# Kernel optimization log

Hardware: AMD Instinct MI355X
Metric: run time of the kernel (lower is better)

Reference implementation:

```python
import jax, jax.numpy as jnp
import numpy as np

KS = 3      # kernel_size
PAD = 1     # zero padding applied to x before sampling
STRIDE = 1  # stride of p_conv and final conv (as written in the repo)


def conv2d(x, w, b=None, stride=1, padding=0):
    out = jax.lax.conv_general_dilated(
        x, w, (stride, stride), [(padding, padding), (padding, padding)],
        dimension_numbers=("NCHW", "OIHW", "NCHW"))
    if b is not None:
        out = out + b[None, :, None, None]
    return out


def setup_inputs() -> dict:
    key = jax.random.key(0)
    k1, k2, k3, k4 = jax.random.split(key, 4)
    bsz, inc, outc, H, W = 4, 64, 128, 128, 128
    N = KS * KS
    x = jax.random.normal(k1, (bsz, inc, H, W), dtype=jnp.float32)
    # p_conv: Conv2d(inc, 2*ks*ks, 3, padding=1) with bias (small weights -> modest offsets)
    w_p = jax.random.normal(k2, (2 * N, inc, 3, 3), dtype=jnp.float32) * 0.02
    b_p = jax.random.normal(k3, (2 * N,), dtype=jnp.float32) * 0.1
    # final conv: Conv2d(inc, outc, ks, stride=stride, bias=None)
    w_conv = jax.random.normal(k4, (outc, inc, KS, KS), dtype=jnp.float32) * 0.05
    return {"x": x, "w_p": w_p, "b_p": b_p, "w_conv": w_conv}


def deform_conv_forward(x, w_p, b_p, w_conv):
    ks, pad, stride = KS, PAD, STRIDE
    offset = conv2d(x, w_p, b_p, stride=stride, padding=1)  # (b, 2N, oh, ow)
    N = offset.shape[1] // 2
    bsz, c, _, _ = x.shape
    oh, ow = offset.shape[2], offset.shape[3]
    xp = jnp.pad(x, ((0, 0), (0, 0), (pad, pad), (pad, pad)))
    Hp, Wp = xp.shape[2], xp.shape[3]

    # p_n: kernel-grid offsets, order matches torch.meshgrid 'ij' then flatten
    r = jnp.arange(-(ks - 1) // 2, (ks - 1) // 2 + 1, dtype=x.dtype)
    pnx, pny = jnp.meshgrid(r, r, indexing="ij")
    p_n = jnp.concatenate([pnx.ravel(), pny.ravel()])[None, :, None, None]  # (1,2N,1,1)

    # p_0: base sampling coordinates (1-indexed into padded image)
    i0 = jnp.arange(1, oh * stride + 1, stride, dtype=x.dtype)
    j0 = jnp.arange(1, ow * stride + 1, stride, dtype=x.dtype)
    p0x = jnp.broadcast_to(i0[:, None], (oh, ow))[None, None]
    p0y = jnp.broadcast_to(j0[None, :], (oh, ow))[None, None]
    p_0 = jnp.concatenate([jnp.tile(p0x, (1, N, 1, 1)), jnp.tile(p0y, (1, N, 1, 1))], axis=1)

    p = (p_0 + p_n + offset).transpose(0, 2, 3, 1)  # (b, oh, ow, 2N)

    q_lt_f = jnp.floor(p)
    q_rb_f = q_lt_f + 1.0

    def clamp_q(q):
        return jnp.concatenate(
            [jnp.clip(q[..., :N], 0, Hp - 1), jnp.clip(q[..., N:], 0, Wp - 1)],
            axis=-1).astype(jnp.int32)

    q_lt = clamp_q(q_lt_f)
    q_rb = clamp_q(q_rb_f)
    q_lb = jnp.concatenate([q_lt[..., :N], q_rb[..., N:]], axis=-1)
    q_rt = jnp.concatenate([q_rb[..., :N], q_lt[..., N:]], axis=-1)

    # clamp p itself (indices are detached in torch; gradients flow only through p here)
    p = jnp.concatenate(
        [jnp.clip(p[..., :N], 0, Hp - 1), jnp.clip(p[..., N:], 0, Wp - 1)], axis=-1)
    px, py = p[..., :N], p[..., N:]

    qf = lambda q: q.astype(x.dtype)
    g_lt = (1 + (qf(q_lt[..., :N]) - px)) * (1 + (qf(q_lt[..., N:]) - py))
    g_rb = (1 - (qf(q_rb[..., :N]) - px)) * (1 - (qf(q_rb[..., N:]) - py))
    g_lb = (1 + (qf(q_lb[..., :N]) - px)) * (1 - (qf(q_lb[..., N:]) - py))
    g_rt = (1 - (qf(q_rt[..., :N]) - px)) * (1 + (qf(q_rt[..., N:]) - py))

    x_flat = xp.reshape(bsz, c, Hp * Wp)

    def get_x_q(q):
        idx = q[..., :N] * Wp + q[..., N:]                     # (b, oh, ow, N)
        idxf = jnp.broadcast_to(idx.reshape(bsz, 1, -1), (bsz, c, oh * ow * N))
        return jnp.take_along_axis(x_flat, idxf, axis=2).reshape(bsz, c, oh, ow, N)

    x_off = (g_lt[:, None] * get_x_q(q_lt) + g_rb[:, None] * get_x_q(q_rb)
             + g_lb[:, None] * get_x_q(q_lb) + g_rt[:, None] * get_x_q(q_rt))

    # _reshape_x_offset: (b,c,oh,ow,ks*ks) -> (b,c,oh*ks,ow*ks)
    x_off = x_off.reshape(bsz, c, oh, ow, ks, ks).transpose(0, 1, 2, 4, 3, 5)
    x_off = x_off.reshape(bsz, c, oh * ks, ow * ks)

    return conv2d(x_off, w_conv, None, stride=stride, padding=0)


def reference(x, w_p, b_p, w_conv):
    return deform_conv_forward(x, w_p, b_p, w_conv)
```

## Files before the change

kernel.cpp:

```cpp
#include <hip/hip_runtime.h>
#include <hip/hip_bf16.h>

#define B_   4
#define IC   64
#define OC   128
#define HH   128
#define WW   128
#define HP   130
#define XOF  384
#define XPAD 388
#define OH2  382

typedef __attribute__((ext_vector_type(4))) float f32x4;
typedef __attribute__((ext_vector_type(8))) __bf16 bf16x8;
typedef __attribute__((ext_vector_type(8))) unsigned short us8;
typedef __attribute__((ext_vector_type(4), aligned(4))) float f32x4u;

__device__ __forceinline__ void gload16(const void* gsrc, void* ldst) {
    __builtin_amdgcn_global_load_lds(
        (const __attribute__((address_space(1))) void*)gsrc,
        (__attribute__((address_space(3))) void*)ldst, 16, 0, 0);
}

#define WAITV(N) asm volatile("s_waitcnt vmcnt(" #N ")" ::: "memory")

__global__ __launch_bounds__(256) void nchw2nhwc(const float* __restrict__ x,
                                                 float* __restrict__ xt) {
    __shared__ float tile[64][33];
    int bid = blockIdx.x;
    int xt4 = bid & 3;
    int y   = (bid >> 2) & 127;
    int b   = bid >> 9;
    int x0  = xt4 * 32;

    int t  = threadIdx.x;
    int xl = t & 31;
    int c8 = t >> 5;
#pragma unroll
    for (int it = 0; it < 8; ++it) {
        int c = it * 8 + c8;
        tile[c][xl] = x[(((size_t)b * IC + c) * HH + y) * WW + x0 + xl];
    }
    __syncthreads();
    int c  = t & 63;
    int xw = t >> 6;
#pragma unroll
    for (int it = 0; it < 8; ++it) {
        int xx = it * 4 + xw;
        xt[(((size_t)b * HH + y) * WW + x0 + xx) * IC + c] = tile[c][xx];
    }
}

__global__ __launch_bounds__(256) void offset_lds4(const float* __restrict__ x,
                                                   const float* __restrict__ w_p,
                                                   const float* __restrict__ b_p,
                                                   float* __restrict__ off) {
    __shared__ float part[4][64][18];

    int t   = threadIdx.x;
    int pxl = t & 63;
    int icq = t >> 6;
    int seg = blockIdx.x & 1;
    int row = blockIdx.x >> 1;
    int py  = row & 127;
    int b   = row >> 7;
    int px  = seg * 64 + pxl;
    int ic0 = __builtin_amdgcn_readfirstlane(icq << 4);

    float acc[18];
#pragma unroll
    for (int co = 0; co < 18; ++co) acc[co] = 0.f;

    const float* xb = x + ((size_t)b * IC + ic0) * HH * WW;

    for (int ci = 0; ci < 16; ++ci) {
        const float* xc = xb + (size_t)ci * HH * WW;
        float xv[9];
#pragma unroll
        for (int ky = 0; ky < 3; ++ky) {
            int yy = py + ky - 1;
            bool yok = (yy >= 0) && (yy < HH);
#pragma unroll
            for (int kx = 0; kx < 3; ++kx) {
                int xx = px + kx - 1;
                bool ok = yok && (xx >= 0) && (xx < WW);
                xv[ky * 3 + kx] = ok ? xc[yy * WW + xx] : 0.f;
            }
        }
#pragma unroll
        for (int co = 0; co < 18; ++co) {
            const float* wrow = w_p + ((size_t)co * IC + ic0 + ci) * 9;
            f32x4u w0 = *(const f32x4u*)wrow;
            f32x4u w1 = *(const f32x4u*)(wrow + 4);
            float  w8 = wrow[8];
            acc[co] = fmaf(w0.x, xv[0], acc[co]);
            acc[co] = fmaf(w0.y, xv[1], acc[co]);
            acc[co] = fmaf(w0.z, xv[2], acc[co]);
            acc[co] = fmaf(w0.w, xv[3], acc[co]);
            acc[co] = fmaf(w1.x, xv[4], acc[co]);
            acc[co] = fmaf(w1.y, xv[5], acc[co]);
            acc[co] = fmaf(w1.z, xv[6], acc[co]);
            acc[co] = fmaf(w1.w, xv[7], acc[co]);
            acc[co] = fmaf(w8,   xv[8], acc[co]);
        }
    }

#pragma unroll
    for (int co = 0; co < 18; ++co) part[icq][pxl][co] = acc[co];
    __syncthreads();

    for (int co = icq; co < 18; co += 4) {
        float s = b_p[co] + part[0][pxl][co] + part[1][pxl][co]
                          + part[2][pxl][co] + part[3][pxl][co];
        off[((size_t)b * 18 + co) * HH * WW + (size_t)py * WW + px] = s;
    }
}

__global__ __launch_bounds__(256) void prep_w(const float* __restrict__ wc,
                                              unsigned short* __restrict__ Bt) {
    int t = blockIdx.x * 256 + threadIdx.x;
    if (t >= 18 * 4 * 128 * 8) return;
    int e  = t & 7;
    int oc = (t >> 3) & 127;
    int kg = (t >> 10) & 3;
    int s  = t >> 12;
    int ic = ((s & 1) << 5) + (kg << 3) + e;
    int kpos = s >> 1;
    int ky = kpos / 3, kx = kpos % 3;
    float v = wc[(((size_t)oc * IC + ic) * 3 + ky) * 3 + kx];
    __hip_bfloat16 h = __float2bfloat16(v);
    Bt[t] = reinterpret_cast<unsigned short&>(h);
}

__global__ __launch_bounds__(256) void sample_nhwc(const float* __restrict__ xt,
                                                   const float* __restrict__ off,
                                                   unsigned short* __restrict__ xoff,
                                                   int b0, int nwg) {
    int orig = blockIdx.x;
    int chunk = nwg >> 3;
    int wg = (orig & 7) * chunk + (orig >> 3);

    int xtile = wg % 12;
    int tmp = wg / 12;
    int yy  = tmp % XOF;
    int bl  = tmp / XOF;
    int b   = b0 + bl;
    int xx0 = xtile * 32;

    int t  = threadIdx.x;
    int xl = t & 31;
    int cg = t >> 5;
    int xx = xx0 + xl;

    int j = xx / 3, kw = xx % 3;
    int i = yy / 3, kh = yy % 3;
    int n = kh * 3 + kw;

    const float* offb = off + (size_t)b * 18 * HH * WW + (size_t)i * WW + j;
    float offr = offb[(size_t)n * HH * WW];
    float offc = offb[(size_t)(n + 9) * HH * WW];

    float pr = (float)(i + kh) + offr;
    float pc = (float)(j + kw) + offc;

    float r0f = floorf(pr), c0f = floorf(pc);
    int r0 = min(max((int)r0f, 0), HP - 1);
    int c0 = min(max((int)c0f, 0), HP - 1);
    int r1 = min(max((int)(r0f + 1.f), 0), HP - 1);
    int c1 = min(max((int)(c0f + 1.f), 0), HP - 1);

    float prc = fminf(fmaxf(pr, 0.f), (float)(HP - 1));
    float pcc = fminf(fmaxf(pc, 0.f), (float)(HP - 1));

    float R0 = 1.f + ((float)r0 - prc);
    float R1 = 1.f - ((float)r1 - prc);
    float C0 = 1.f + ((float)c0 - pcc);
    float C1 = 1.f - ((float)c1 - pcc);

    int rr0 = r0 - 1, cc0 = c0 - 1, rr1 = r1 - 1, cc1 = c1 - 1;
    if (!(rr0 >= 0 && rr0 < HH)) R0 = 0.f;
    if (!(rr1 >= 0 && rr1 < HH)) R1 = 0.f;
    float C0m = (cc0 >= 0 && cc0 < WW) ? C0 : 0.f;
    float C1m = (cc1 >= 0 && cc1 < WW) ? C1 : 0.f;
    int ra0 = min(max(rr0, 0), HH - 1);
    int ra1 = min(max(rr1, 0), HH - 1);
    int ca0 = min(max(cc0, 0), WW - 1);
    int ca1 = min(max(cc1, 0), WW - 1);

    const float* xb = xt + (size_t)b * HH * WW * IC + cg * 8;
    const float* p00 = xb + ((size_t)ra0 * WW + ca0) * IC;
    const float* p01 = xb + ((size_t)ra0 * WW + ca1) * IC;
    const float* p10 = xb + ((size_t)ra1 * WW + ca0) * IC;
    const float* p11 = xb + ((size_t)ra1 * WW + ca1) * IC;

    us8 res;
#pragma unroll
    for (int h = 0; h < 2; ++h) {
        f32x4u a  = *(const f32x4u*)(p00 + h * 4);
        f32x4u bb = *(const f32x4u*)(p01 + h * 4);
        f32x4u cc = *(const f32x4u*)(p10 + h * 4);
        f32x4u dd = *(const f32x4u*)(p11 + h * 4);
#pragma unroll
        for (int e = 0; e < 4; ++e) {
            float v = R0 * (C0m * a[e] + C1m * bb[e]) +
                      R1 * (C0m * cc[e] + C1m * dd[e]);
            __hip_bfloat16 hh = __float2bfloat16(v);
            res[h * 4 + e] = reinterpret_cast<unsigned short&>(hh);
        }
    }

    size_t di = ((((size_t)bl * XOF + yy) * 8 + cg) * XPAD + xx) * 8;
    *(us8*)(xoff + di) = res;
}

__global__ __launch_bounds__(256) void conv2_mfma(const unsigned short* __restrict__ xoff,
                                                  const unsigned short* __restrict__ Bt,
                                                  float* __restrict__ out,
                                                  int b0, int nwg) {
    __shared__ __align__(16) char lds[40960];

    int orig = blockIdx.x;
    int q = nwg >> 3, r = nwg & 7;
    int xcd = orig & 7, loc = orig >> 3;
    int wgid = (xcd < r ? xcd * (q + 1) : r * (q + 1) + (xcd - r) * q) + loc;

    int xt  = wgid % 3;
    int tmp = wgid / 3;
    int oy  = tmp % OH2;
    int bl  = tmp / OH2;
    int x0  = xt << 7;

    int tid  = threadIdx.x;
    int wave = tid >> 6, lane = tid & 63;
    int wm = wave >> 1;
    int wn = wave & 1;
    int lr = lane & 15, lc = lane >> 4;

    const char* xb = (const char*)xoff + (size_t)bl * ((size_t)XOF * 8 * XPAD * 16);
    const char* bt = (const char*)Bt;

    f32x4 acc[4][4];
#pragma unroll
    for (int mf = 0; mf < 4; ++mf)
#pragma unroll
        for (int nf = 0; nf < 4; ++nf)
            acc[mf][nf] = (f32x4){0.f, 0.f, 0.f, 0.f};

    auto stageA = [&](int abuf, int s6, int third) {
        int ky  = s6 >> 1;
        int ich = s6 & 1;
        int L   = third * 4 + wave;
        int cg  = L / 3, seg = L % 3;
        const char* src = xb +
            (((size_t)(oy + ky) * 8 + ich * 4 + cg) * XPAD + x0 + seg * 64 + lane) * 16;
        char* dst = lds + abuf * 12288 + (cg * 192 + seg * 64) * 16;
        gload16(src, dst);
    };
    auto stageA_full = [&](int abuf, int s6) {
#pragma unroll
        for (int qq = 0; qq < 3; ++qq) {
            int ky  = s6 >> 1;
            int ich = s6 & 1;
            int L   = wave * 3 + qq;
            int cg  = L / 3, seg = L % 3;
            const char* src = xb +
                (((size_t)(oy + ky) * 8 + ich * 4 + cg) * XPAD + x0 + seg * 64 + lane) * 16;
            char* dst = lds + abuf * 12288 + (cg * 192 + seg * 64) * 16;
            gload16(src, dst);
        }
    };
    auto stageB = [&](int bbuf, int t) {
        int s6 = t / 3, kx = t % 3;
        int sB = ((s6 >> 1) * 3 + kx) * 2 + (s6 & 1);
        const char* bsrc = bt + (size_t)sB * 8192;
#pragma unroll
        for (int g2 = 0; g2 < 2; ++g2) {
            int g = wave * 2 + g2;
            gload16(bsrc + (size_t)g * 1024 + lane * 16,
                    lds + 24576 + bbuf * 8192 + g * 1024);
        }
    };

    auto compute = [&](int abuf, int bbuf, int kx) {
        const char* abase = lds + abuf * 12288;
        const char* bbase = lds + 24576 + bbuf * 8192;
        bf16x8 af[4], bfr[4];
#pragma unroll
        for (int mf = 0; mf < 4; ++mf)
            af[mf] = *(const bf16x8*)(abase +
                (lc * 192 + wm * 64 + mf * 16 + lr + kx) * 16);
#pragma unroll
        for (int nf = 0; nf < 4; ++nf)
            bfr[nf] = *(const bf16x8*)(bbase +
                (lc * 128 + wn * 64 + nf * 16 + lr) * 16);
#pragma unroll
        for (int mf = 0; mf < 4; ++mf)
#pragma unroll
            for (int nf = 0; nf < 4; ++nf)
                acc[mf][nf] = __builtin_amdgcn_mfma_f32_16x16x32_bf16(
                    af[mf], bfr[nf], acc[mf][nf], 0, 0, 0);
    };

    stageA_full(0, 0);
    stageB(0, 0);

    int abuf = 0, bbuf = 0;
#pragma unroll
    for (int s6 = 0; s6 < 6; ++s6) {
#pragma unroll
        for (int kx = 0; kx < 3; ++kx) {
            const int t = s6 * 3 + kx;
            if (t + 1 < 18) stageB(bbuf ^ 1, t + 1);
            if (s6 + 1 < 6) stageA(abuf ^ 1, s6 + 1, kx);
            if (s6 < 5)          { WAITV(3); }
            else if (kx < 2)     { WAITV(2); }
            else                 { WAITV(0); }
            __builtin_amdgcn_s_barrier();
            __builtin_amdgcn_sched_barrier(0);
            compute(abuf, bbuf, kx);
            __builtin_amdgcn_sched_barrier(0);
            __builtin_amdgcn_s_barrier();
            bbuf ^= 1;
        }
        abuf ^= 1;
    }

    int b = b0 + bl;
#pragma unroll
    for (int mf = 0; mf < 4; ++mf) {
        int ox0 = x0 + wm * 64 + mf * 16 + (lc << 2);
#pragma unroll
        for (int nf = 0; nf < 4; ++nf) {
            int oc = wn * 64 + nf * 16 + lr;
            float* po = out + (((size_t)b * OC + oc) * OH2 + oy) * OH2 + ox0;
            if (ox0 + 3 < OH2) {
                *(f32x4u*)po = acc[mf][nf];
            } else {
#pragma unroll
                for (int rr = 0; rr < 4; ++rr)
                    if (ox0 + rr < OH2) po[rr] = acc[mf][nf][rr];
            }
        }
    }
}

extern "C" void kernel_launch(void* const* d_in, const int* in_sizes, int n_in,
                              void* d_out, int out_size, void* d_ws, size_t ws_size,
                              hipStream_t stream) {
    const float* x      = (const float*)d_in[0];
    const float* w_p    = (const float*)d_in[1];
    const float* b_p    = (const float*)d_in[2];
    const float* w_conv = (const float*)d_in[3];
    float* out = (float*)d_out;

    const size_t offElems = (size_t)B_ * 18 * HH * WW;
    const size_t xtElems  = (size_t)B_ * HH * WW * IC;
    const size_t btElems  = (size_t)18 * 4 * 128 * 8;
    const size_t xofElems = (size_t)XOF * 8 * XPAD * 8;
    const size_t slack    = 16384;

    float* off = (float*)d_ws;
    float* xtb = off + offElems;
    unsigned short* Bt   = (unsigned short*)(xtb + xtElems);
    unsigned short* xoff = Bt + btElems;

    const size_t headBytes = (offElems + xtElems) * 4 + btElems * 2;
    const bool allBatch = ws_size >= headBytes + 4 * xofElems * 2 + slack;

    prep_w<<<(int)((btElems + 255) / 256), 256, 0, stream>>>(w_conv, Bt);
    nchw2nhwc<<<2048, 256, 0, stream>>>(x, xtb);
    offset_lds4<<<1024, 256, 0, stream>>>(x, w_p, b_p, off);

    if (allBatch) {
        int snwg = 12 * XOF * B_;
        sample_nhwc<<<snwg, 256, 0, stream>>>(xtb, off, xoff, 0, snwg);
        int cnwg = 3 * OH2 * B_;
        conv2_mfma<<<cnwg, 256, 0, stream>>>(xoff, Bt, out, 0, cnwg);
    } else {
        for (int b = 0; b < B_; ++b) {
            int snwg = 12 * XOF;
            sample_nhwc<<<snwg, 256, 0, stream>>>(xtb, off, xoff, b, snwg);
            int cnwg = 3 * OH2;
            conv2_mfma<<<cnwg, 256, 0, stream>>>(xoff, Bt, out, b, cnwg);
        }
    }
}
```

Before: 249.3 us.

## Fuse prologue kernels, store NHWC input as bf16, raise MFMA wave priority

Merges the weight prep, NCHW-to-NHWC transpose and offset conv into one launch, with each block range doing a different job. The transposed input is now stored as bf16, which halves the transpose write traffic and the sampler's gather bytes; the sampler loads 8 bf16 values per corner in one vector load. Wave priority is raised around the MFMA block in the conv kernel. Rounding the input to bf16 before bilinear interpolation adds an extra rounding step, which slightly changes numerics.

```diff
diff --git a/kernel.cpp b/kernel.cpp
--- a/kernel.cpp
+++ b/kernel.cpp
@@ -24,115 +24,122 @@
 
 #define WAITV(N) asm volatile("s_waitcnt vmcnt(" #N ")" ::: "memory")
 
-__global__ __launch_bounds__(256) void nchw2nhwc(const float* __restrict__ x,
-                                                 float* __restrict__ xt) {
-    __shared__ float tile[64][33];
+__device__ __forceinline__ float bf2f(unsigned short u) {
+    union { unsigned int i; float f; } v; v.i = ((unsigned int)u) << 16; return v.f;
+}
+__device__ __forceinline__ unsigned short f2bf(float f) {
+    __hip_bfloat16 h = __float2bfloat16(f);
+    return reinterpret_cast<unsigned short&>(h);
+}
+
+__global__ __launch_bounds__(256) void prologue(const float* __restrict__ x,
+                                                const float* __restrict__ w_p,
+                                                const float* __restrict__ b_p,
+                                                const float* __restrict__ wc,
+                                                float* __restrict__ off,
+                                                unsigned short* __restrict__ xt,
+                                                unsigned short* __restrict__ Bt) {
+    __shared__ __align__(16) char smem[18432];
     int bid = blockIdx.x;
-    int xt4 = bid & 3;
-    int y   = (bid >> 2) & 127;
-    int b   = bid >> 9;
-    int x0  = xt4 * 32;
-
-    int t  = threadIdx.x;
-    int xl = t & 31;
-    int c8 = t >> 5;
-#pragma unroll
-    for (int it = 0; it < 8; ++it) {
-        int c = it * 8 + c8;
-        tile[c][xl] = x[(((size_t)b * IC + c) * HH + y) * WW + x0 + xl];
-    }
-    __syncthreads();
-    int c  = t & 63;
-    int xw = t >> 6;
-#pragma unroll
-    for (int it = 0; it < 8; ++it) {
-        int xx = it * 4 + xw;
-        xt[(((size_t)b * HH + y) * WW + x0 + xx) * IC + c] = tile[c][xx];
-    }
-}
-
-__global__ __launch_bounds__(256) void offset_lds4(const float* __restrict__ x,
-                                                   const float* __restrict__ w_p,
-                                                   const float* __restrict__ b_p,
-                                                   float* __restrict__ off) {
-    __shared__ float part[4][64][18];
-
-    int t   = threadIdx.x;
-    int pxl = t & 63;
-    int icq = t >> 6;
-    int seg = blockIdx.x & 1;
-    int row = blockIdx.x >> 1;
-    int py  = row & 127;
-    int b   = row >> 7;
-    int px  = seg * 64 + pxl;
-    int ic0 = __builtin_amdgcn_readfirstlane(icq << 4);
-
-    float acc[18];
-#pragma unroll
-    for (int co = 0; co < 18; ++co) acc[co] = 0.f;
-
-    const float* xb = x + ((size_t)b * IC + ic0) * HH * WW;
-
-    for (int ci = 0; ci < 16; ++ci) {
-        const float* xc = xb + (size_t)ci * HH * WW;
-        float xv[9];
-#pragma unroll
-        for (int ky = 0; ky < 3; ++ky) {
-            int yy = py + ky - 1;
-            bool yok = (yy >= 0) && (yy < HH);
-#pragma unroll
-            for (int kx = 0; kx < 3; ++kx) {
-                int xx = px + kx - 1;
-                bool ok = yok && (xx >= 0) && (xx < WW);
-                xv[ky * 3 + kx] = ok ? xc[yy * WW + xx] : 0.f;
+    int tid = threadIdx.x;
+
+    if (bid < 2048) {
+        unsigned short (*tile)[34] = (unsigned short(*)[34])smem;
+        int xt4 = bid & 3;
+        int y   = (bid >> 2) & 127;
+        int b   = bid >> 9;
+        int x0  = xt4 * 32;
+
+        int xl = tid & 31;
+        int c8 = tid >> 5;
+#pragma unroll
+        for (int it = 0; it < 8; ++it) {
+            int c = it * 8 + c8;
+            tile[c][xl] = f2bf(x[(((size_t)b * IC + c) * HH + y) * WW + x0 + xl]);
+        }
+        __syncthreads();
+        int c2 = (tid & 31) * 2;
+#pragma unroll
+        for (int it = 0; it < 4; ++it) {
+            int xx = (tid >> 5) + it * 8;
+            ushort2 v = { tile[c2][xx], tile[c2 + 1][xx] };
+            *(ushort2*)(xt + (((size_t)b * HH + y) * WW + x0 + xx) * IC + c2) = v;
+        }
+    } else if (bid < 3072) {
+        float (*part)[64][18] = (float(*)[64][18])smem;
+        int obid = bid - 2048;
+        int pxl = tid & 63;
+        int icq = tid >> 6;
+        int seg = obid & 1;
+        int row = obid >> 1;
+        int py  = row & 127;
+        int b   = row >> 7;
+        int px  = seg * 64 + pxl;
+        int ic0 = __builtin_amdgcn_readfirstlane(icq << 4);
+
+        float acc[18];
+#pragma unroll
+        for (int co = 0; co < 18; ++co) acc[co] = 0.f;
+
+        const float* xb = x + ((size_t)b * IC + ic0) * HH * WW;
+
+        for (int ci = 0; ci < 16; ++ci) {
+            const float* xc = xb + (size_t)ci * HH * WW;
+            float xv[9];
+#pragma unroll
+            for (int ky = 0; ky < 3; ++ky) {
+                int yy = py + ky - 1;
+                bool yok = (yy >= 0) && (yy < HH);
+#pragma unroll
+                for (int kx = 0; kx < 3; ++kx) {
+                    int xx = px + kx - 1;
+                    bool ok = yok && (xx >= 0) && (xx < WW);
+                    xv[ky * 3 + kx] = ok ? xc[yy * WW + xx] : 0.f;
+                }
             }
-        }
-#pragma unroll
-        for (int co = 0; co < 18; ++co) {
-            const float* wrow = w_p + ((size_t)co * IC + ic0 + ci) * 9;
-            f32x4u w0 = *(const f32x4u*)wrow;
-            f32x4u w1 = *(const f32x4u*)(wrow + 4);
-            float  w8 = wrow[8];
-            acc[co] = fmaf(w0.x, xv[0], acc[co]);
-            acc[co] = fmaf(w0.y, xv[1], acc[co]);
-            acc[co] = fmaf(w0.z, xv[2], acc[co]);
-            acc[co] = fmaf(w0.w, xv[3], acc[co]);
-            acc[co] = fmaf(w1.x, xv[4], acc[co]);
-            acc[co] = fmaf(w1.y, xv[5], acc[co]);
-            acc[co] = fmaf(w1.z, xv[6], acc[co]);
-            acc[co] = fmaf(w1.w, xv[7], acc[co]);
-            acc[co] = fmaf(w8,   xv[8], acc[co]);
-        }
-    }
-
-#pragma unroll
-    for (int co = 0; co < 18; ++co) part[icq][pxl][co] = acc[co];
-    __syncthreads();
-
-    for (int co = icq; co < 18; co += 4) {
-        float s = b_p[co] + part[0][pxl][co] + part[1][pxl][co]
-                          + part[2][pxl][co] + part[3][pxl][co];
-        off[((size_t)b * 18 + co) * HH * WW + (size_t)py * WW + px] = s;
-    }
-}
-
-__global__ __launch_bounds__(256) void prep_w(const float* __restrict__ wc,
-                                              unsigned short* __restrict__ Bt) {
-    int t = blockIdx.x * 256 + threadIdx.x;
-    if (t >= 18 * 4 * 128 * 8) return;
-    int e  = t & 7;
-    int oc = (t >> 3) & 127;
-    int kg = (t >> 10) & 3;
-    int s  = t >> 12;
-    int ic = ((s & 1) << 5) + (kg << 3) + e;
-    int kpos = s >> 1;
-    int ky = kpos / 3, kx = kpos % 3;
-    float v = wc[(((size_t)oc * IC + ic) * 3 + ky) * 3 + kx];
-    __hip_bfloat16 h = __float2bfloat16(v);
-    Bt[t] = reinterpret_cast<unsigned short&>(h);
-}
-
-__global__ __launch_bounds__(256) void sample_nhwc(const float* __restrict__ xt,
+#pragma unroll
+            for (int co = 0; co < 18; ++co) {
+                const float* wrow = w_p + ((size_t)co * IC + ic0 + ci) * 9;
+                f32x4u w0 = *(const f32x4u*)wrow;
+                f32x4u w1 = *(const f32x4u*)(wrow + 4);
+                float  w8 = wrow[8];
+                acc[co] = fmaf(w0.x, xv[0], acc[co]);
+                acc[co] = fmaf(w0.y, xv[1], acc[co]);
+                acc[co] = fmaf(w0.z, xv[2], acc[co]);
+                acc[co] = fmaf(w0.w, xv[3], acc[co]);
+                acc[co] = fmaf(w1.x, xv[4], acc[co]);
+                acc[co] = fmaf(w1.y, xv[5], acc[co]);
+                acc[co] = fmaf(w1.z, xv[6], acc[co]);
+                acc[co] = fmaf(w1.w, xv[7], acc[co]);
+                acc[co] = fmaf(w8,   xv[8], acc[co]);
+            }
+        }
+
+#pragma unroll
+        for (int co = 0; co < 18; ++co) part[icq][pxl][co] = acc[co];
+        __syncthreads();
+
+        for (int co = icq; co < 18; co += 4) {
+            float s = b_p[co] + part[0][pxl][co] + part[1][pxl][co]
+                              + part[2][pxl][co] + part[3][pxl][co];
+            off[((size_t)b * 18 + co) * HH * WW + (size_t)py * WW + px] = s;
+        }
+    } else {
+        int t = (bid - 3072) * 256 + tid;
+        if (t < 18 * 4 * 128 * 8) {
+            int e  = t & 7;
+            int oc = (t >> 3) & 127;
+            int kg = (t >> 10) & 3;
+            int s  = t >> 12;
+            int ic = ((s & 1) << 5) + (kg << 3) + e;
+            int kpos = s >> 1;
+            int ky = kpos / 3, kx = kpos % 3;
+            Bt[t] = f2bf(wc[(((size_t)oc * IC + ic) * 3 + ky) * 3 + kx]);
+        }
+    }
+}
+
+__global__ __launch_bounds__(256) void sample_nhwc(const unsigned short* __restrict__ xt,
                                                    const float* __restrict__ off,
                                                    unsigned short* __restrict__ xoff,
                                                    int b0, int nwg) {
@@ -187,26 +194,18 @@
     int ca0 = min(max(cc0, 0), WW - 1);
     int ca1 = min(max(cc1, 0), WW - 1);
 
-    const float* xb = xt + (size_t)b * HH * WW * IC + cg * 8;
-    const float* p00 = xb + ((size_t)ra0 * WW + ca0) * IC;
-    const float* p01 = xb + ((size_t)ra0 * WW + ca1) * IC;
-    const float* p10 = xb + ((size_t)ra1 * WW + ca0) * IC;
-    const float* p11 = xb + ((size_t)ra1 * WW + ca1) * IC;
+    const unsigned short* xb = xt + (size_t)b * HH * WW * IC + cg * 8;
+    us8 a  = *(const us8*)(xb + ((size_t)ra0 * WW + ca0) * IC);
+    us8 bb = *(const us8*)(xb + ((size_t)ra0 * WW + ca1) * IC);
+    us8 cc = *(const us8*)(xb + ((size_t)ra1 * WW + ca0) * IC);
+    us8 dd = *(const us8*)(xb + ((size_t)ra1 * WW + ca1) * IC);
 
     us8 res;
 #pragma unroll
-    for (int h = 0; h < 2; ++h) {
-        f32x4u a  = *(const f32x4u*)(p00 + h * 4);
-        f32x4u bb = *(const f32x4u*)(p01 + h * 4);
-        f32x4u cc = *(const f32x4u*)(p10 + h * 4);
-        f32x4u dd = *(const f32x4u*)(p11 + h * 4);
-#pragma unroll
-        for (int e = 0; e < 4; ++e) {
-            float v = R0 * (C0m * a[e] + C1m * bb[e]) +
-                      R1 * (C0m * cc[e] + C1m * dd[e]);
-            __hip_bfloat16 hh = __float2bfloat16(v);
-            res[h * 4 + e] = reinterpret_cast<unsigned short&>(hh);
-        }
+    for (int e = 0; e < 8; ++e) {
+        float v = R0 * (C0m * bf2f(a[e]) + C1m * bf2f(bb[e])) +
+                  R1 * (C0m * bf2f(cc[e]) + C1m * bf2f(dd[e]));
+        res[e] = f2bf(v);
     }
 
     size_t di = ((((size_t)bl * XOF + yy) * 8 + cg) * XPAD + xx) * 8;
@@ -293,12 +292,14 @@
         for (int nf = 0; nf < 4; ++nf)
             bfr[nf] = *(const bf16x8*)(bbase +
                 (lc * 128 + wn * 64 + nf * 16 + lr) * 16);
+        __builtin_amdgcn_s_setprio(1);
 #pragma unroll
         for (int mf = 0; mf < 4; ++mf)
 #pragma unroll
             for (int nf = 0; nf < 4; ++nf)
                 acc[mf][nf] = __builtin_amdgcn_mfma_f32_16x16x32_bf16(
                     af[mf], bfr[nf], acc[mf][nf], 0, 0, 0);
+        __builtin_amdgcn_s_setprio(0);
     };
 
     stageA_full(0, 0);
@@ -360,16 +361,14 @@
     const size_t slack    = 16384;
 
     float* off = (float*)d_ws;
-    float* xtb = off + offElems;
-    unsigned short* Bt   = (unsigned short*)(xtb + xtElems);
+    unsigned short* xtb  = (unsigned short*)(off + offElems);
+    unsigned short* Bt   = xtb + xtElems;
     unsigned short* xoff = Bt + btElems;
 
-    const size_t headBytes = (offElems + xtElems) * 4 + btElems * 2;
+    const size_t headBytes = offElems * 4 + (xtElems + btElems) * 2;
     const bool allBatch = ws_size >= headBytes + 4 * xofElems * 2 + slack;
 
-    prep_w<<<(int)((btElems + 255) / 256), 256, 0, stream>>>(w_conv, Bt);
-    nchw2nhwc<<<2048, 256, 0, stream>>>(x, xtb);
-    offset_lds4<<<1024, 256, 0, stream>>>(x, w_p, b_p, off);
+    prologue<<<3360, 256, 0, stream>>>(x, w_p, b_p, w_conv, off, xtb, Bt);
 
     if (allBatch) {
         int snwg = 12 * XOF * B_;
```

Result: faster. 228.5 us (-8.4%).
